# Kernel tuning notes

Measured on AMD Instinct MI355X. Metric: run time of the kernel, lower is better.

Reference implementation:

```python
import jax, jax.numpy as jnp
import numpy as np

B, S, F = 16, 128, 64          # batch, seq_len, feature_dim
H = 256                        # hidden_dim
HEADS = 4
DH = H // HEADS                # GAT per-head dim = 64
AH = (2 * H) // HEADS          # temporal-attn head dim = 128
N = 1024                       # num graph nodes (edge_index.max()+1)
E = 16384                      # num edges (avg degree 16)
D2 = 2 * H                     # bi-LSTM output dim = 512
BN_INV = 1.0 / np.sqrt(1.0 + 1e-5)   # eval-mode BatchNorm1d (running mean=0, var=1)


def lstm_dir(x_sf, Wih, Whh, bih, bhh):
    # x_sf: [S, B, F]; torch gate order i, f, g, o
    h0 = jnp.zeros((x_sf.shape[1], Whh.shape[1]), x_sf.dtype)
    def step(carry, xt):
        h, c = carry
        z = xt @ Wih.T + h @ Whh.T + bih + bhh
        i, f, g, o = jnp.split(z, 4, axis=-1)
        c = jax.nn.sigmoid(f) * c + jax.nn.sigmoid(i) * jnp.tanh(g)
        h = jax.nn.sigmoid(o) * jnp.tanh(c)
        return (h, c), h
    _, hs = jax.lax.scan(step, (h0, h0), x_sf)
    return hs


def setup_inputs():
    key = jax.random.key(0)
    ks = jax.random.split(key, 32)
    g = lambda i, sh: jax.random.normal(ks[i], sh, jnp.float32) * 0.05
    return {
        "x": jax.random.normal(ks[0], (B, S, F), jnp.float32),
        "edge_index": jax.random.randint(ks[1], (2, E), 0, N),
        "Wih_f": g(2, (4 * H, F)), "Whh_f": g(3, (4 * H, H)),
        "bih_f": g(4, (4 * H,)), "bhh_f": g(5, (4 * H,)),
        "Wih_b": g(6, (4 * H, F)), "Whh_b": g(7, (4 * H, H)),
        "bih_b": g(8, (4 * H,)), "bhh_b": g(9, (4 * H,)),
        "Wq": g(10, (D2, D2)), "bq": g(11, (D2,)),
        "Wk": g(12, (D2, D2)), "bk": g(13, (D2,)),
        "Wv": g(14, (D2, D2)), "bv": g(15, (D2,)),
        "Wo": g(16, (D2, D2)), "bo": g(17, (D2,)),
        "W1": g(18, (D2, H)), "a1s": g(19, (HEADS, DH)), "a1d": g(20, (HEADS, DH)), "b1": g(21, (H,)),
        "g1": jnp.ones((H,), jnp.float32), "be1": jnp.zeros((H,), jnp.float32),
        "W2": g(22, (H, H)), "a2s": g(23, (HEADS, DH)), "a2d": g(24, (HEADS, DH)), "b2": g(25, (H,)),
        "g2": jnp.ones((H,), jnp.float32), "be2": jnp.zeros((H,), jnp.float32),
        "Wf": g(26, (H, 3 * H)), "bf": g(27, (H,)),
        "ln_g": jnp.ones((H,), jnp.float32), "ln_b": jnp.zeros((H,), jnp.float32),
    }


def reference(x, edge_index, Wih_f, Whh_f, bih_f, bhh_f, Wih_b, Whh_b, bih_b, bhh_b,
              Wq, bq, Wk, bk, Wv, bv, Wo, bo,
              W1, a1s, a1d, b1, g1, be1, W2, a2s, a2d, b2, g2, be2,
              Wf, bf, ln_g, ln_b):
    # ---- bidirectional LSTM ----
    xs = jnp.swapaxes(x, 0, 1)                                   # [S,B,F]
    hf = lstm_dir(xs, Wih_f, Whh_f, bih_f, bhh_f)
    hb = jnp.flip(lstm_dir(jnp.flip(xs, 0), Wih_b, Whh_b, bih_b, bhh_b), 0)
    t = jnp.swapaxes(jnp.concatenate([hf, hb], -1), 0, 1)        # [B,S,2H]
    # ---- temporal multi-head attention ----
    def proj(W, b):
        return (t @ W.T + b).reshape(B, S, HEADS, AH).transpose(0, 2, 1, 3)
    Q, K, V = proj(Wq, bq), proj(Wk, bk), proj(Wv, bv)
    scores = jnp.einsum('bhqd,bhkd->bhqk', Q, K) / np.sqrt(AH)
    attn = jax.nn.softmax(scores, -1)                            # [B,HEADS,S,S]
    ao = jnp.einsum('bhqk,bhkd->bhqd', attn, V).transpose(0, 2, 1, 3).reshape(B, S, D2)
    last = (ao @ Wo.T + bo)[:, -1, :]                            # [B,2H]
    # ---- 2-layer GAT per sample (PyG GATConv, add_self_loops=True), vmapped over batch ----
    loops = jnp.arange(N)
    src = jnp.concatenate([edge_index[0], loops])
    dst = jnp.concatenate([edge_index[1], loops])
    def gat(h_in, W, a_s, a_d, b):
        h = (h_in @ W).reshape(N, HEADS, DH)
        e = jax.nn.leaky_relu((h * a_s).sum(-1)[src] + (h * a_d).sum(-1)[dst], 0.2)  # [Etot,HEADS]
        m = jax.ops.segment_max(e, dst, num_segments=N)
        w = jnp.exp(e - m[dst])
        z = jax.ops.segment_sum(w, dst, num_segments=N)
        alpha = w / (z[dst] + 1e-16)
        out = jax.ops.segment_sum(alpha[:, :, None] * h[src], dst, num_segments=N)
        return out.reshape(N, H) + b
    def spatial(v):
        feat = jnp.broadcast_to(v, (N, D2))                      # uniform node features, per original
        h1 = jax.nn.elu(gat(feat, W1, a1s, a1d, b1) * BN_INV * g1 + be1)
        h2 = jax.nn.elu(gat(h1, W2, a2s, a2d, b2) * BN_INV * g2 + be2)
        return h2.mean(0)
    sp = jax.vmap(spatial)(last)                                 # [B,H]
    # ---- fusion: Linear + LayerNorm + ReLU (dropout = eval no-op) ----
    f = jnp.concatenate([last, sp], -1) @ Wf.T + bf
    mu = f.mean(-1, keepdims=True)
    var = ((f - mu) ** 2).mean(-1, keepdims=True)
    fused = jax.nn.relu((f - mu) / jnp.sqrt(var + 1e-5) * ln_g + ln_b)
    return fused, attn
```

## Files before the change

### kernel.cpp

```cpp
#include <hip/hip_runtime.h>


typedef unsigned short u16;
typedef unsigned int u32;
typedef __bf16 bf16x8 __attribute__((ext_vector_type(8)));
typedef float f32x4 __attribute__((ext_vector_type(4)));
typedef unsigned short ushort8v __attribute__((ext_vector_type(8)));
typedef unsigned int uint4v __attribute__((ext_vector_type(4)));

#define BN_INV_F 0.9999950000374997f
#define POISON 0xFFFFFFFFu

__device__ __forceinline__ float b2f(u16 u) {
  union { float f; unsigned int i; } v;
  v.i = ((unsigned int)u) << 16;
  return v.f;
}
__device__ __forceinline__ u16 f2b(float f) {
  union { float f; unsigned int i; } v;
  v.f = f;
  unsigned int x = v.i;
  unsigned int r = (x + 0x7FFFu + ((x >> 16) & 1u)) >> 16;
  return (u16)r;
}
__device__ __forceinline__ f32x4 mfma16(ushort8v a, ushort8v b, f32x4 c) {
  return __builtin_amdgcn_mfma_f32_16x16x32_bf16(
      __builtin_bit_cast(bf16x8, a), __builtin_bit_cast(bf16x8, b), c, 0, 0, 0);
}
__device__ __forceinline__ float sigm(float x) { return 1.f / (1.f + __expf(-x)); }
__device__ __forceinline__ float tanh_f(float x) {
  float e = __expf(2.f * x);
  return 1.f - 2.f / (e + 1.f);
}

__global__ __launch_bounds__(256) void lstm_kernel(
    const float* __restrict__ x,
    const float* __restrict__ Wih0, const float* __restrict__ Whh0,
    const float* __restrict__ bih0, const float* __restrict__ bhh0,
    const float* __restrict__ Wih1, const float* __restrict__ Whh1,
    const float* __restrict__ bih1, const float* __restrict__ bhh1,
    u32* __restrict__ hbuf,
    u16* __restrict__ tb)
{
  const int tid = threadIdx.x;
  const int bx = blockIdx.x;
  const int d = bx >> 4;
  const int q = bx & 15;
  const float* Wih = d ? Wih1 : Wih0;
  const float* Whh = d ? Whh1 : Whh0;
  const float* bih = d ? bih1 : bih0;
  const float* bhh = d ? bhh1 : bhh0;

  __shared__ u16 whh_s[64][264];
  __shared__ u16 wih_s[64][72];
  __shared__ u16 h_s[16][264];
  __shared__ u16 x_s[16][72];
  __shared__ float z_s[4][16][17];
  __shared__ float bias_s[64];

  {
    int r = tid >> 2, seg = tid & 3;
    int grow = ((r >> 4) << 8) + q * 16 + (r & 15);
    const float4* src = (const float4*)(Whh + grow * 256 + seg * 64);
#pragma unroll
    for (int i = 0; i < 16; i++) {
      float4 v = src[i];
      whh_s[r][seg * 64 + i * 4 + 0] = f2b(v.x);
      whh_s[r][seg * 64 + i * 4 + 1] = f2b(v.y);
      whh_s[r][seg * 64 + i * 4 + 2] = f2b(v.z);
      whh_s[r][seg * 64 + i * 4 + 3] = f2b(v.w);
    }
    const float4* src2 = (const float4*)(Wih + grow * 64 + seg * 16);
#pragma unroll
    for (int i = 0; i < 4; i++) {
      float4 v = src2[i];
      wih_s[r][seg * 16 + i * 4 + 0] = f2b(v.x);
      wih_s[r][seg * 16 + i * 4 + 1] = f2b(v.y);
      wih_s[r][seg * 16 + i * 4 + 2] = f2b(v.z);
      wih_s[r][seg * 16 + i * 4 + 3] = f2b(v.w);
    }
  }
  if (tid < 64) {
    int grow = ((tid >> 4) << 8) + q * 16 + (tid & 15);
    bias_s[tid] = bih[grow] + bhh[grow];
  }

  const int w = tid >> 6;
  const int ln = tid & 63;
  const int col16 = ln & 15;
  const int quad = ln >> 4;
  const int eb = tid >> 4;
  const int ec = tid & 15;
  float c_reg = 0.f;

  for (int t = 0; t < 128; t++) {
    const int pos = d ? (127 - t) : t;
    {
      int b_ = tid >> 4;
      int f0 = (tid & 15) * 4;
      float4 xv = *(const float4*)(x + (b_ * 128 + pos) * 64 + f0);
      x_s[b_][f0 + 0] = f2b(xv.x);
      x_s[b_][f0 + 1] = f2b(xv.y);
      x_s[b_][f0 + 2] = f2b(xv.z);
      x_s[b_][f0 + 3] = f2b(xv.w);
    }
    if (t > 0) {
      const u32* hw = hbuf + (t * 2 + d) * 2048 + tid * 8;
      uint4v a, b;
      for (;;) {
        asm volatile(
            "global_load_dwordx4 %0, %2, off sc1\n\t"
            "global_load_dwordx4 %1, %3, off sc1\n\t"
            "s_waitcnt vmcnt(0)"
            : "=v"(a), "=v"(b)
            : "v"(hw), "v"(hw + 4)
            : "memory");
        bool ok = (a.x != POISON) & (a.y != POISON) & (a.z != POISON) &
                  (a.w != POISON) & (b.x != POISON) & (b.y != POISON) &
                  (b.z != POISON) & (b.w != POISON);
        if (ok) break;
      }
      int b_ = tid >> 4, c0 = (tid & 15) * 16;
      *(u32*)&h_s[b_][c0 + 0] = a.x;
      *(u32*)&h_s[b_][c0 + 2] = a.y;
      *(u32*)&h_s[b_][c0 + 4] = a.z;
      *(u32*)&h_s[b_][c0 + 6] = a.w;
      *(u32*)&h_s[b_][c0 + 8] = b.x;
      *(u32*)&h_s[b_][c0 + 10] = b.y;
      *(u32*)&h_s[b_][c0 + 12] = b.z;
      *(u32*)&h_s[b_][c0 + 14] = b.w;
    }
    __syncthreads();

    f32x4 acc = {0.f, 0.f, 0.f, 0.f};
#pragma unroll
    for (int kt = 0; kt < 2; kt++) {
      ushort8v av = *(const ushort8v*)&x_s[col16][kt * 32 + quad * 8];
      ushort8v bv = *(const ushort8v*)&wih_s[w * 16 + col16][kt * 32 + quad * 8];
      acc = mfma16(av, bv, acc);
    }
    if (t > 0) {
#pragma unroll
      for (int kt = 0; kt < 8; kt++) {
        ushort8v av = *(const ushort8v*)&h_s[col16][kt * 32 + quad * 8];
        ushort8v bv = *(const ushort8v*)&whh_s[w * 16 + col16][kt * 32 + quad * 8];
        acc = mfma16(av, bv, acc);
      }
    }
#pragma unroll
    for (int reg = 0; reg < 4; reg++)
      z_s[w][quad * 4 + reg][col16] = acc[reg];
    __syncthreads();

    float zi = z_s[0][eb][ec] + bias_s[ec];
    float zf = z_s[1][eb][ec] + bias_s[16 + ec];
    float zg = z_s[2][eb][ec] + bias_s[32 + ec];
    float zo = z_s[3][eb][ec] + bias_s[48 + ec];
    float si = sigm(zi), sf = sigm(zf), so = sigm(zo);
    float tg = tanh_f(zg);
    c_reg = sf * c_reg + si * tg;
    float hv = so * tanh_f(c_reg);
    u32 my = (u32)f2b(hv);
    u32 hi = __shfl_down((int)my, 1);
    if ((ec & 1) == 0) {
      u32 word = my | (hi << 16);
      *(u32*)&tb[(eb * 128 + pos) * 512 + d * 256 + q * 16 + ec] = word;
      if (t < 127) {
        u32* dst = hbuf + ((t + 1) * 2 + d) * 2048 + eb * 128 + (q * 16 + ec) / 2;
        __hip_atomic_store(dst, word, __ATOMIC_RELAXED,
                           __HIP_MEMORY_SCOPE_AGENT);
      }
    }
  }
}

__global__ __launch_bounds__(256) void qkv_kernel(
    const u16* __restrict__ tb,
    const float* __restrict__ Wq, const float* __restrict__ bq,
    const float* __restrict__ Wk, const float* __restrict__ bk,
    const float* __restrict__ Wv, const float* __restrict__ bv,
    u16* __restrict__ Qb, u16* __restrict__ Kb, u16* __restrict__ Vb)
{
  const int tid = threadIdx.x;
  const int bxm = blockIdx.x, byn = blockIdx.y, bz = blockIdx.z;
  const float* W = (bz == 0) ? Wq : ((bz == 1) ? Wk : Wv);
  const float* bias = (bz == 0) ? bq : ((bz == 1) ? bk : bv);
  u16* outp = (bz == 0) ? Qb : ((bz == 1) ? Kb : Vb);

  __shared__ u16 a_s[64][40];
  __shared__ u16 b_s[64][40];
  const int w = tid >> 6, ln = tid & 63, col16 = ln & 15, quad = ln >> 4;

  f32x4 acc[4];
#pragma unroll
  for (int n = 0; n < 4; n++) acc[n] = (f32x4){0.f, 0.f, 0.f, 0.f};

  for (int kt = 0; kt < 16; kt++) {
    int r = tid >> 2, seg = tid & 3;
    *(ushort8v*)&a_s[r][seg * 8] =
        *(const ushort8v*)(tb + (bxm * 64 + r) * 512 + kt * 32 + seg * 8);
    const float4* wsrc = (const float4*)(W + (byn * 64 + r) * 512 + kt * 32 + seg * 8);
    float4 w0 = wsrc[0], w1 = wsrc[1];
    b_s[r][seg * 8 + 0] = f2b(w0.x);
    b_s[r][seg * 8 + 1] = f2b(w0.y);
    b_s[r][seg * 8 + 2] = f2b(w0.z);
    b_s[r][seg * 8 + 3] = f2b(w0.w);
    b_s[r][seg * 8 + 4] = f2b(w1.x);
    b_s[r][seg * 8 + 5] = f2b(w1.y);
    b_s[r][seg * 8 + 6] = f2b(w1.z);
    b_s[r][seg * 8 + 7] = f2b(w1.w);
    __syncthreads();
    ushort8v av = *(const ushort8v*)&a_s[w * 16 + col16][quad * 8];
#pragma unroll
    for (int n = 0; n < 4; n++) {
      ushort8v bvv = *(const ushort8v*)&b_s[n * 16 + col16][quad * 8];
      acc[n] = mfma16(av, bvv, acc[n]);
    }
    __syncthreads();
  }
#pragma unroll
  for (int n = 0; n < 4; n++) {
    float bs = bias[byn * 64 + n * 16 + col16];
#pragma unroll
    for (int reg = 0; reg < 4; reg++) {
      int row = bxm * 64 + w * 16 + quad * 4 + reg;
      outp[row * 512 + byn * 64 + n * 16 + col16] = f2b(acc[n][reg] + bs);
    }
  }
}

__global__ __launch_bounds__(256) void attn_kernel(
    const u16* __restrict__ Qb, const u16* __restrict__ Kb,
    float* __restrict__ attn_out)
{
  const int b = blockIdx.x, h = blockIdx.y, half = blockIdx.z;
  const int tid = threadIdx.x;
  __shared__ __align__(16) char smem[52224];
  u16 (*q_s)[136] = (u16(*)[136])smem;
  u16 (*k_s)[136] = (u16(*)[136])(smem + 17408);
  float (*sc)[132] = (float(*)[132])smem;

  const int w = tid >> 6, ln = tid & 63, col16 = ln & 15, quad = ln >> 4;
  {
    int r = tid >> 2, seg = tid & 3;
    const u16* src = Qb + (b * 128 + half * 64 + r) * 512 + h * 128 + seg * 32;
#pragma unroll
    for (int i = 0; i < 4; i++)
      *(ushort8v*)&q_s[r][seg * 32 + i * 8] = *(const ushort8v*)(src + i * 8);
    int r2 = tid >> 1, sg = tid & 1;
    const u16* src2 = Kb + (b * 128 + r2) * 512 + h * 128 + sg * 64;
#pragma unroll
    for (int i = 0; i < 8; i++)
      *(ushort8v*)&k_s[r2][sg * 64 + i * 8] = *(const ushort8v*)(src2 + i * 8);
  }
  __syncthreads();

  f32x4 acc[8];
#pragma unroll
  for (int n = 0; n < 8; n++) acc[n] = (f32x4){0.f, 0.f, 0.f, 0.f};
#pragma unroll
  for (int kd = 0; kd < 4; kd++) {
    ushort8v av = *(const ushort8v*)&q_s[w * 16 + col16][kd * 32 + quad * 8];
#pragma unroll
    for (int n = 0; n < 8; n++) {
      ushort8v bvv = *(const ushort8v*)&k_s[n * 16 + col16][kd * 32 + quad * 8];
      acc[n] = mfma16(av, bvv, acc[n]);
    }
  }
  __syncthreads();
  const float scale = 0.08838834764831845f;
#pragma unroll
  for (int n = 0; n < 8; n++)
#pragma unroll
    for (int reg = 0; reg < 4; reg++)
      sc[w * 16 + quad * 4 + reg][n * 16 + col16] = acc[n][reg] * scale;
  __syncthreads();

  const int row = tid >> 2, p = tid & 3;
  float m = -1e30f;
  for (int c0 = 0; c0 < 32; c0++) m = fmaxf(m, sc[row][p * 32 + c0]);
  m = fmaxf(m, __shfl_xor(m, 1));
  m = fmaxf(m, __shfl_xor(m, 2));
  float s = 0.f;
  for (int c0 = 0; c0 < 32; c0++) {
    float e = __expf(sc[row][p * 32 + c0] - m);
    sc[row][p * 32 + c0] = e;
    s += e;
  }
  s += __shfl_xor(s, 1);
  s += __shfl_xor(s, 2);
  float inv = 1.f / s;
  float* orow = attn_out + ((b * 4 + h) * 128 + half * 64 + row) * 128 + p * 32;
  for (int c0 = 0; c0 < 32; c0++) orow[c0] = sc[row][p * 32 + c0] * inv;
}

__global__ __launch_bounds__(256) void tail_kernel(
    const float* __restrict__ attn, const u16* __restrict__ Vb,
    const float* __restrict__ Wo, const float* __restrict__ bo,
    const float* __restrict__ W1, const float* __restrict__ b1,
    const float* __restrict__ g1, const float* __restrict__ be1,
    const float* __restrict__ W2, const float* __restrict__ pb2,
    const float* __restrict__ g2, const float* __restrict__ be2,
    const float* __restrict__ Wf, const float* __restrict__ bfv,
    const float* __restrict__ ln_g, const float* __restrict__ ln_b,
    float* __restrict__ dout)
{
  const int b = blockIdx.x, tid = threadIdx.x;
  __shared__ float arow[4][128];
  __shared__ float ao_s[512];
  __shared__ float last_s[512];
  __shared__ float h_s2[256];
  __shared__ float red_s[4];

#pragma unroll
  for (int e = 0; e < 2; e++) {
    int idx = tid + e * 256;
    int h = idx >> 7, k = idx & 127;
    arow[h][k] = attn[((b * 4 + h) * 128 + 127) * 128 + k];
  }
  __syncthreads();
#pragma unroll
  for (int pass = 0; pass < 2; pass++) {
    int d2 = tid + pass * 256;
    int hh = d2 >> 7;
    float acc = 0.f;
    for (int k = 0; k < 128; k++)
      acc += arow[hh][k] * b2f(Vb[(b * 128 + k) * 512 + d2]);
    ao_s[d2] = acc;
  }
  __syncthreads();
#pragma unroll
  for (int pass = 0; pass < 2; pass++) {
    int j = tid + pass * 256;
    float acc = bo[j];
    const float4* Wo4 = (const float4*)(Wo + j * 512);
    for (int k4 = 0; k4 < 128; k4++) {
      float4 wv = Wo4[k4];
      acc += ao_s[k4 * 4 + 0] * wv.x + ao_s[k4 * 4 + 1] * wv.y +
             ao_s[k4 * 4 + 2] * wv.z + ao_s[k4 * 4 + 3] * wv.w;
    }
    last_s[j] = acc;
  }
  __syncthreads();

  const int j = tid;
  float acc = 0.f;
  for (int k = 0; k < 512; k++) acc += last_s[k] * W1[k * 256 + j];
  float u = (acc + b1[j]) * BN_INV_F * g1[j] + be1[j];
  float h1 = u > 0.f ? u : expm1f(u);
  h_s2[j] = h1;
  __syncthreads();

  float acc2 = 0.f;
  for (int k = 0; k < 256; k++) acc2 += h_s2[k] * W2[k * 256 + j];
  float u2 = (acc2 + pb2[j]) * BN_INV_F * g2[j] + be2[j];
  float sp = u2 > 0.f ? u2 : expm1f(u2);
  __syncthreads();
  h_s2[j] = sp;
  __syncthreads();

  float f = bfv[j];
  const float4* Wf4 = (const float4*)(Wf + j * 768);
  for (int k4 = 0; k4 < 128; k4++) {
    float4 wv = Wf4[k4];
    f += last_s[k4 * 4 + 0] * wv.x + last_s[k4 * 4 + 1] * wv.y +
         last_s[k4 * 4 + 2] * wv.z + last_s[k4 * 4 + 3] * wv.w;
  }
  for (int k4 = 0; k4 < 64; k4++) {
    float4 wv = Wf4[128 + k4];
    f += h_s2[k4 * 4 + 0] * wv.x + h_s2[k4 * 4 + 1] * wv.y +
         h_s2[k4 * 4 + 2] * wv.z + h_s2[k4 * 4 + 3] * wv.w;
  }

  float v = f;
#pragma unroll
  for (int o = 32; o > 0; o >>= 1) v += __shfl_xor(v, o);
  if ((tid & 63) == 0) red_s[tid >> 6] = v;
  __syncthreads();
  float mu = (red_s[0] + red_s[1] + red_s[2] + red_s[3]) * (1.f / 256.f);
  float dv = f - mu;
  float vv = dv * dv;
#pragma unroll
  for (int o = 32; o > 0; o >>= 1) vv += __shfl_xor(vv, o);
  __syncthreads();
  if ((tid & 63) == 0) red_s[tid >> 6] = vv;
  __syncthreads();
  float var = (red_s[0] + red_s[1] + red_s[2] + red_s[3]) * (1.f / 256.f);
  float y = dv * rsqrtf(var + 1e-5f) * ln_g[j] + ln_b[j];
  dout[b * 256 + j] = fmaxf(y, 0.f);
}

extern "C" void kernel_launch(void* const* d_in, const int* in_sizes, int n_in,
                              void* d_out, int out_size, void* d_ws, size_t ws_size,
                              hipStream_t stream) {
  (void)in_sizes; (void)n_in; (void)out_size; (void)ws_size;
  const float* x     = (const float*)d_in[0];
  const float* Wih_f = (const float*)d_in[2];
  const float* Whh_f = (const float*)d_in[3];
  const float* bih_f = (const float*)d_in[4];
  const float* bhh_f = (const float*)d_in[5];
  const float* Wih_b = (const float*)d_in[6];
  const float* Whh_b = (const float*)d_in[7];
  const float* bih_b = (const float*)d_in[8];
  const float* bhh_b = (const float*)d_in[9];
  const float* Wq = (const float*)d_in[10]; const float* bq = (const float*)d_in[11];
  const float* Wk = (const float*)d_in[12]; const float* bk = (const float*)d_in[13];
  const float* Wv = (const float*)d_in[14]; const float* bv = (const float*)d_in[15];
  const float* Wo = (const float*)d_in[16]; const float* bo = (const float*)d_in[17];
  const float* W1 = (const float*)d_in[18];
  const float* b1 = (const float*)d_in[21];
  const float* g1 = (const float*)d_in[22]; const float* be1 = (const float*)d_in[23];
  const float* W2 = (const float*)d_in[24];
  const float* pb2 = (const float*)d_in[27];
  const float* g2 = (const float*)d_in[28]; const float* be2 = (const float*)d_in[29];
  const float* Wf = (const float*)d_in[30]; const float* bfv = (const float*)d_in[31];
  const float* ln_g = (const float*)d_in[32]; const float* ln_b = (const float*)d_in[33];

  float* dout = (float*)d_out;
  char* ws = (char*)d_ws;
  u32* hbuf = (u32*)(ws + 0);
  u16* tb   = (u16*)(ws + 2129920);
  u16* Qb   = (u16*)(ws + 4227072);
  u16* Kb   = (u16*)(ws + 6324224);
  u16* Vb   = (u16*)(ws + 8421376);

  (void)hipMemsetAsync(ws, 0xFF, 2097152, stream);
  lstm_kernel<<<32, 256, 0, stream>>>(x, Wih_f, Whh_f, bih_f, bhh_f,
                                      Wih_b, Whh_b, bih_b, bhh_b,
                                      hbuf, tb);
  qkv_kernel<<<dim3(32, 8, 3), 256, 0, stream>>>(tb, Wq, bq, Wk, bk, Wv, bv,
                                                 Qb, Kb, Vb);
  attn_kernel<<<dim3(16, 4, 2), 256, 0, stream>>>(Qb, Kb, dout + 4096);
  tail_kernel<<<16, 256, 0, stream>>>(dout + 4096, Vb, Wo, bo,
                                      W1, b1, g1, be1, W2, pb2, g2, be2,
                                      Wf, bfv, ln_g, ln_b, dout);
}
```

Measured before the change: 441.2 us.

## Keep LSTM weights in registers and drop shared memory and barriers per step

```diff
diff --git a/kernel.cpp b/kernel.cpp
--- a/kernel.cpp
+++ b/kernel.cpp
@@ -32,6 +32,7 @@
   float e = __expf(2.f * x);
   return 1.f - 2.f / (e + 1.f);
 }
+__device__ __forceinline__ u32 umaxu(u32 a, u32 b) { return a > b ? a : b; }
 
 __global__ __launch_bounds__(256) void lstm_kernel(
     const float* __restrict__ x,
@@ -51,124 +52,130 @@
   const float* bih = d ? bih1 : bih0;
   const float* bhh = d ? bhh1 : bhh0;
 
-  __shared__ u16 whh_s[64][264];
-  __shared__ u16 wih_s[64][72];
-  __shared__ u16 h_s[16][264];
-  __shared__ u16 x_s[16][72];
-  __shared__ float z_s[4][16][17];
-  __shared__ float bias_s[64];
-
-  {
-    int r = tid >> 2, seg = tid & 3;
-    int grow = ((r >> 4) << 8) + q * 16 + (r & 15);
-    const float4* src = (const float4*)(Whh + grow * 256 + seg * 64);
-#pragma unroll
-    for (int i = 0; i < 16; i++) {
-      float4 v = src[i];
-      whh_s[r][seg * 64 + i * 4 + 0] = f2b(v.x);
-      whh_s[r][seg * 64 + i * 4 + 1] = f2b(v.y);
-      whh_s[r][seg * 64 + i * 4 + 2] = f2b(v.z);
-      whh_s[r][seg * 64 + i * 4 + 3] = f2b(v.w);
-    }
-    const float4* src2 = (const float4*)(Wih + grow * 64 + seg * 16);
-#pragma unroll
-    for (int i = 0; i < 4; i++) {
-      float4 v = src2[i];
-      wih_s[r][seg * 16 + i * 4 + 0] = f2b(v.x);
-      wih_s[r][seg * 16 + i * 4 + 1] = f2b(v.y);
-      wih_s[r][seg * 16 + i * 4 + 2] = f2b(v.z);
-      wih_s[r][seg * 16 + i * 4 + 3] = f2b(v.w);
-    }
-  }
-  if (tid < 64) {
-    int grow = ((tid >> 4) << 8) + q * 16 + (tid & 15);
-    bias_s[tid] = bih[grow] + bhh[grow];
-  }
-
   const int w = tid >> 6;
   const int ln = tid & 63;
   const int col16 = ln & 15;
   const int quad = ln >> 4;
-  const int eb = tid >> 4;
-  const int ec = tid & 15;
-  float c_reg = 0.f;
+
+  const int G = (col16 >> 2) * 256 + q * 16 + w * 4 + (col16 & 3);
+
+  ushort8v whh_f[8];
+#pragma unroll
+  for (int kt = 0; kt < 8; kt++) {
+    const float4* src = (const float4*)(Whh + G * 256 + kt * 32 + quad * 8);
+    float4 v0 = src[0], v1 = src[1];
+    ushort8v t8;
+    t8[0] = f2b(v0.x); t8[1] = f2b(v0.y); t8[2] = f2b(v0.z); t8[3] = f2b(v0.w);
+    t8[4] = f2b(v1.x); t8[5] = f2b(v1.y); t8[6] = f2b(v1.z); t8[7] = f2b(v1.w);
+    whh_f[kt] = t8;
+  }
+  ushort8v wih_f[2];
+#pragma unroll
+  for (int kt = 0; kt < 2; kt++) {
+    const float4* src = (const float4*)(Wih + G * 64 + kt * 32 + quad * 8);
+    float4 v0 = src[0], v1 = src[1];
+    ushort8v t8;
+    t8[0] = f2b(v0.x); t8[1] = f2b(v0.y); t8[2] = f2b(v0.z); t8[3] = f2b(v0.w);
+    t8[4] = f2b(v1.x); t8[5] = f2b(v1.y); t8[6] = f2b(v1.z); t8[7] = f2b(v1.w);
+    wih_f[kt] = t8;
+  }
+  const float bias = bih[G] + bhh[G];
+
+  f32x4 c_reg = {0.f, 0.f, 0.f, 0.f};
+  const int colbase = q * 16 + w * 4 + col16;
 
   for (int t = 0; t < 128; t++) {
     const int pos = d ? (127 - t) : t;
+
+    ushort8v ax0, ax1;
     {
-      int b_ = tid >> 4;
-      int f0 = (tid & 15) * 4;
-      float4 xv = *(const float4*)(x + (b_ * 128 + pos) * 64 + f0);
-      x_s[b_][f0 + 0] = f2b(xv.x);
-      x_s[b_][f0 + 1] = f2b(xv.y);
-      x_s[b_][f0 + 2] = f2b(xv.z);
-      x_s[b_][f0 + 3] = f2b(xv.w);
-    }
+      const float4* xs = (const float4*)(x + (col16 * 128 + pos) * 64 + quad * 8);
+      float4 v0 = xs[0], v1 = xs[1];
+      const float4* xs1 = (const float4*)(x + (col16 * 128 + pos) * 64 + 32 + quad * 8);
+      float4 v2 = xs1[0], v3 = xs1[1];
+      ax0[0] = f2b(v0.x); ax0[1] = f2b(v0.y); ax0[2] = f2b(v0.z); ax0[3] = f2b(v0.w);
+      ax0[4] = f2b(v1.x); ax0[5] = f2b(v1.y); ax0[6] = f2b(v1.z); ax0[7] = f2b(v1.w);
+      ax1[0] = f2b(v2.x); ax1[1] = f2b(v2.y); ax1[2] = f2b(v2.z); ax1[3] = f2b(v2.w);
+      ax1[4] = f2b(v3.x); ax1[5] = f2b(v3.y); ax1[6] = f2b(v3.z); ax1[7] = f2b(v3.w);
+    }
+    f32x4 acc = {0.f, 0.f, 0.f, 0.f};
+    acc = mfma16(ax0, wih_f[0], acc);
+    acc = mfma16(ax1, wih_f[1], acc);
+
     if (t > 0) {
-      const u32* hw = hbuf + (t * 2 + d) * 2048 + tid * 8;
-      uint4v a, b;
+      const u32* hb = hbuf + (t * 2 + d) * 2048 + col16 * 128 + quad * 4;
+      uint4v p0, p1, p2, p3, p4, p5, p6, p7;
       for (;;) {
         asm volatile(
-            "global_load_dwordx4 %0, %2, off sc1\n\t"
-            "global_load_dwordx4 %1, %3, off sc1\n\t"
+            "global_load_dwordx4 %0, %8, off sc1\n\t"
+            "global_load_dwordx4 %1, %8, off offset:64 sc1\n\t"
+            "global_load_dwordx4 %2, %8, off offset:128 sc1\n\t"
+            "global_load_dwordx4 %3, %8, off offset:192 sc1\n\t"
+            "global_load_dwordx4 %4, %8, off offset:256 sc1\n\t"
+            "global_load_dwordx4 %5, %8, off offset:320 sc1\n\t"
+            "global_load_dwordx4 %6, %8, off offset:384 sc1\n\t"
+            "global_load_dwordx4 %7, %8, off offset:448 sc1\n\t"
             "s_waitcnt vmcnt(0)"
-            : "=v"(a), "=v"(b)
-            : "v"(hw), "v"(hw + 4)
+            : "=v"(p0), "=v"(p1), "=v"(p2), "=v"(p3),
+              "=v"(p4), "=v"(p5), "=v"(p6), "=v"(p7)
+            : "v"(hb)
             : "memory");
-        bool ok = (a.x != POISON) & (a.y != POISON) & (a.z != POISON) &
-                  (a.w != POISON) & (b.x != POISON) & (b.y != POISON) &
-                  (b.z != POISON) & (b.w != POISON);
-        if (ok) break;
+        u32 mx = p0.x;
+        mx = umaxu(mx, p0.y); mx = umaxu(mx, p0.z); mx = umaxu(mx, p0.w);
+        mx = umaxu(mx, p1.x); mx = umaxu(mx, p1.y); mx = umaxu(mx, p1.z); mx = umaxu(mx, p1.w);
+        mx = umaxu(mx, p2.x); mx = umaxu(mx, p2.y); mx = umaxu(mx, p2.z); mx = umaxu(mx, p2.w);
+        mx = umaxu(mx, p3.x); mx = umaxu(mx, p3.y); mx = umaxu(mx, p3.z); mx = umaxu(mx, p3.w);
+        mx = umaxu(mx, p4.x); mx = umaxu(mx, p4.y); mx = umaxu(mx, p4.z); mx = umaxu(mx, p4.w);
+        mx = umaxu(mx, p5.x); mx = umaxu(mx, p5.y); mx = umaxu(mx, p5.z); mx = umaxu(mx, p5.w);
+        mx = umaxu(mx, p6.x); mx = umaxu(mx, p6.y); mx = umaxu(mx, p6.z); mx = umaxu(mx, p6.w);
+        mx = umaxu(mx, p7.x); mx = umaxu(mx, p7.y); mx = umaxu(mx, p7.z); mx = umaxu(mx, p7.w);
+        if (mx != POISON) break;
       }
-      int b_ = tid >> 4, c0 = (tid & 15) * 16;
-      *(u32*)&h_s[b_][c0 + 0] = a.x;
-      *(u32*)&h_s[b_][c0 + 2] = a.y;
-      *(u32*)&h_s[b_][c0 + 4] = a.z;
-      *(u32*)&h_s[b_][c0 + 6] = a.w;
-      *(u32*)&h_s[b_][c0 + 8] = b.x;
-      *(u32*)&h_s[b_][c0 + 10] = b.y;
-      *(u32*)&h_s[b_][c0 + 12] = b.z;
-      *(u32*)&h_s[b_][c0 + 14] = b.w;
-    }
-    __syncthreads();
-
-    f32x4 acc = {0.f, 0.f, 0.f, 0.f};
-#pragma unroll
-    for (int kt = 0; kt < 2; kt++) {
-      ushort8v av = *(const ushort8v*)&x_s[col16][kt * 32 + quad * 8];
-      ushort8v bv = *(const ushort8v*)&wih_s[w * 16 + col16][kt * 32 + quad * 8];
-      acc = mfma16(av, bv, acc);
-    }
-    if (t > 0) {
-#pragma unroll
-      for (int kt = 0; kt < 8; kt++) {
-        ushort8v av = *(const ushort8v*)&h_s[col16][kt * 32 + quad * 8];
-        ushort8v bv = *(const ushort8v*)&whh_s[w * 16 + col16][kt * 32 + quad * 8];
-        acc = mfma16(av, bv, acc);
-      }
-    }
-#pragma unroll
-    for (int reg = 0; reg < 4; reg++)
-      z_s[w][quad * 4 + reg][col16] = acc[reg];
-    __syncthreads();
-
-    float zi = z_s[0][eb][ec] + bias_s[ec];
-    float zf = z_s[1][eb][ec] + bias_s[16 + ec];
-    float zg = z_s[2][eb][ec] + bias_s[32 + ec];
-    float zo = z_s[3][eb][ec] + bias_s[48 + ec];
-    float si = sigm(zi), sf = sigm(zf), so = sigm(zo);
-    float tg = tanh_f(zg);
-    c_reg = sf * c_reg + si * tg;
-    float hv = so * tanh_f(c_reg);
-    u32 my = (u32)f2b(hv);
-    u32 hi = __shfl_down((int)my, 1);
-    if ((ec & 1) == 0) {
-      u32 word = my | (hi << 16);
-      *(u32*)&tb[(eb * 128 + pos) * 512 + d * 256 + q * 16 + ec] = word;
-      if (t < 127) {
-        u32* dst = hbuf + ((t + 1) * 2 + d) * 2048 + eb * 128 + (q * 16 + ec) / 2;
-        __hip_atomic_store(dst, word, __ATOMIC_RELAXED,
-                           __HIP_MEMORY_SCOPE_AGENT);
+      acc = mfma16(__builtin_bit_cast(ushort8v, p0), whh_f[0], acc);
+      acc = mfma16(__builtin_bit_cast(ushort8v, p1), whh_f[1], acc);
+      acc = mfma16(__builtin_bit_cast(ushort8v, p2), whh_f[2], acc);
+      acc = mfma16(__builtin_bit_cast(ushort8v, p3), whh_f[3], acc);
+      acc = mfma16(__builtin_bit_cast(ushort8v, p4), whh_f[4], acc);
+      acc = mfma16(__builtin_bit_cast(ushort8v, p5), whh_f[5], acc);
+      acc = mfma16(__builtin_bit_cast(ushort8v, p6), whh_f[6], acc);
+      acc = mfma16(__builtin_bit_cast(ushort8v, p7), whh_f[7], acc);
+    }
+
+    float zz[4], zf[4], zg[4], zo[4];
+#pragma unroll
+    for (int r = 0; r < 4; r++) zz[r] = acc[r] + bias;
+#pragma unroll
+    for (int r = 0; r < 4; r++) {
+      zf[r] = __shfl_xor(zz[r], 4);
+      zg[r] = __shfl_xor(zz[r], 8);
+      zo[r] = __shfl_xor(zz[r], 12);
+    }
+
+    u32 word[4];
+#pragma unroll
+    for (int r = 0; r < 4; r++) {
+      float si = sigm(zz[r]);
+      float sf = sigm(zf[r]);
+      float so = sigm(zo[r]);
+      float tg = tanh_f(zg[r]);
+      float cc = sf * c_reg[r] + si * tg;
+      c_reg[r] = cc;
+      float hv = so * tanh_f(cc);
+      u32 my = (u32)f2b(hv);
+      u32 hi = ((u32)__shfl_xor((int)my, 1)) & 0xFFFFu;
+      word[r] = my | (hi << 16);
+    }
+
+    if (col16 == 0 || col16 == 2) {
+#pragma unroll
+      for (int r = 0; r < 4; r++) {
+        const int batch = quad * 4 + r;
+        *(u32*)&tb[(batch * 128 + pos) * 512 + d * 256 + colbase] = word[r];
+        if (t < 127) {
+          u32* dst = hbuf + ((t + 1) * 2 + d) * 2048 + batch * 128 + (colbase >> 1);
+          __hip_atomic_store(dst, word[r], __ATOMIC_RELAXED,
+                             __HIP_MEMORY_SCOPE_AGENT);
+        }
       }
     }
   }
```

After: 617.0 us. 1.4x slower.

## Keep LSTM weights in registers, prefetch x early, coalesce attention stores

Applied to the files above, without the earlier changes.

```diff
diff --git a/kernel.cpp b/kernel.cpp
--- a/kernel.cpp
+++ b/kernel.cpp
@@ -51,59 +51,51 @@
   const float* bih = d ? bih1 : bih0;
   const float* bhh = d ? bhh1 : bhh0;
 
-  __shared__ u16 whh_s[64][264];
-  __shared__ u16 wih_s[64][72];
+  const int w = tid >> 6;
+  const int ln = tid & 63;
+  const int col16 = ln & 15;
+  const int quad = ln >> 4;
+
   __shared__ u16 h_s[16][264];
   __shared__ u16 x_s[16][72];
   __shared__ float z_s[4][16][17];
   __shared__ float bias_s[64];
 
-  {
-    int r = tid >> 2, seg = tid & 3;
-    int grow = ((r >> 4) << 8) + q * 16 + (r & 15);
-    const float4* src = (const float4*)(Whh + grow * 256 + seg * 64);
-#pragma unroll
-    for (int i = 0; i < 16; i++) {
-      float4 v = src[i];
-      whh_s[r][seg * 64 + i * 4 + 0] = f2b(v.x);
-      whh_s[r][seg * 64 + i * 4 + 1] = f2b(v.y);
-      whh_s[r][seg * 64 + i * 4 + 2] = f2b(v.z);
-      whh_s[r][seg * 64 + i * 4 + 3] = f2b(v.w);
-    }
-    const float4* src2 = (const float4*)(Wih + grow * 64 + seg * 16);
-#pragma unroll
-    for (int i = 0; i < 4; i++) {
-      float4 v = src2[i];
-      wih_s[r][seg * 16 + i * 4 + 0] = f2b(v.x);
-      wih_s[r][seg * 16 + i * 4 + 1] = f2b(v.y);
-      wih_s[r][seg * 16 + i * 4 + 2] = f2b(v.z);
-      wih_s[r][seg * 16 + i * 4 + 3] = f2b(v.w);
-    }
+  const int G = w * 256 + q * 16 + col16;
+  ushort8v whh_f[8];
+#pragma unroll
+  for (int kt = 0; kt < 8; kt++) {
+    const float4* src = (const float4*)(Whh + G * 256 + kt * 32 + quad * 8);
+    float4 v0 = src[0], v1 = src[1];
+    ushort8v t8;
+    t8[0] = f2b(v0.x); t8[1] = f2b(v0.y); t8[2] = f2b(v0.z); t8[3] = f2b(v0.w);
+    t8[4] = f2b(v1.x); t8[5] = f2b(v1.y); t8[6] = f2b(v1.z); t8[7] = f2b(v1.w);
+    whh_f[kt] = t8;
+  }
+  ushort8v wih_f[2];
+#pragma unroll
+  for (int kt = 0; kt < 2; kt++) {
+    const float4* src = (const float4*)(Wih + G * 64 + kt * 32 + quad * 8);
+    float4 v0 = src[0], v1 = src[1];
+    ushort8v t8;
+    t8[0] = f2b(v0.x); t8[1] = f2b(v0.y); t8[2] = f2b(v0.z); t8[3] = f2b(v0.w);
+    t8[4] = f2b(v1.x); t8[5] = f2b(v1.y); t8[6] = f2b(v1.z); t8[7] = f2b(v1.w);
+    wih_f[kt] = t8;
   }
   if (tid < 64) {
     int grow = ((tid >> 4) << 8) + q * 16 + (tid & 15);
     bias_s[tid] = bih[grow] + bhh[grow];
   }
 
-  const int w = tid >> 6;
-  const int ln = tid & 63;
-  const int col16 = ln & 15;
-  const int quad = ln >> 4;
   const int eb = tid >> 4;
   const int ec = tid & 15;
   float c_reg = 0.f;
 
   for (int t = 0; t < 128; t++) {
     const int pos = d ? (127 - t) : t;
-    {
-      int b_ = tid >> 4;
-      int f0 = (tid & 15) * 4;
-      float4 xv = *(const float4*)(x + (b_ * 128 + pos) * 64 + f0);
-      x_s[b_][f0 + 0] = f2b(xv.x);
-      x_s[b_][f0 + 1] = f2b(xv.y);
-      x_s[b_][f0 + 2] = f2b(xv.z);
-      x_s[b_][f0 + 3] = f2b(xv.w);
-    }
+
+    float4 xv = *(const float4*)(x + (eb * 128 + pos) * 64 + ec * 4);
+
     if (t > 0) {
       const u32* hw = hbuf + (t * 2 + d) * 2048 + tid * 8;
       uint4v a, b;
@@ -130,21 +122,26 @@
       *(u32*)&h_s[b_][c0 + 12] = b.z;
       *(u32*)&h_s[b_][c0 + 14] = b.w;
     }
+    {
+      int f0 = ec * 4;
+      x_s[eb][f0 + 0] = f2b(xv.x);
+      x_s[eb][f0 + 1] = f2b(xv.y);
+      x_s[eb][f0 + 2] = f2b(xv.z);
+      x_s[eb][f0 + 3] = f2b(xv.w);
+    }
     __syncthreads();
 
     f32x4 acc = {0.f, 0.f, 0.f, 0.f};
 #pragma unroll
     for (int kt = 0; kt < 2; kt++) {
       ushort8v av = *(const ushort8v*)&x_s[col16][kt * 32 + quad * 8];
-      ushort8v bv = *(const ushort8v*)&wih_s[w * 16 + col16][kt * 32 + quad * 8];
-      acc = mfma16(av, bv, acc);
+      acc = mfma16(av, wih_f[kt], acc);
     }
     if (t > 0) {
 #pragma unroll
       for (int kt = 0; kt < 8; kt++) {
         ushort8v av = *(const ushort8v*)&h_s[col16][kt * 32 + quad * 8];
-        ushort8v bv = *(const ushort8v*)&whh_s[w * 16 + col16][kt * 32 + quad * 8];
-        acc = mfma16(av, bv, acc);
+        acc = mfma16(av, whh_f[kt], acc);
       }
     }
 #pragma unroll
@@ -236,6 +233,7 @@
   const int b = blockIdx.x, h = blockIdx.y, half = blockIdx.z;
   const int tid = threadIdx.x;
   __shared__ __align__(16) char smem[52224];
+  __shared__ float inv_s[64];
   u16 (*q_s)[136] = (u16(*)[136])smem;
   u16 (*k_s)[136] = (u16(*)[136])(smem + 17408);
   float (*sc)[132] = (float(*)[132])smem;
@@ -289,9 +287,20 @@
   }
   s += __shfl_xor(s, 1);
   s += __shfl_xor(s, 2);
-  float inv = 1.f / s;
-  float* orow = attn_out + ((b * 4 + h) * 128 + half * 64 + row) * 128 + p * 32;
-  for (int c0 = 0; c0 < 32; c0++) orow[c0] = sc[row][p * 32 + c0] * inv;
+  if (p == 0) inv_s[row] = 1.f / s;
+  __syncthreads();
+
+  float* obase = attn_out + (size_t)((b * 4 + h) * 128 + half * 64) * 128;
+#pragma unroll
+  for (int it = 0; it < 8; it++) {
+    int idx = tid + it * 256;
+    int r = idx >> 5;
+    int c4 = idx & 31;
+    float4 ev = *(float4*)&sc[r][c4 * 4];
+    float iv = inv_s[r];
+    float4 ov = {ev.x * iv, ev.y * iv, ev.z * iv, ev.w * iv};
+    *(float4*)&obase[r * 128 + c4 * 4] = ov;
+  }
 }
 
 __global__ __launch_bounds__(256) void tail_kernel(
```

Result: no change. 434.0 us, median of 2 (-1.6%).
